# Kernel tuning notes

Hardware: AMD Instinct MI355X
Metric: run time of the kernel (lower is better)

Reference implementation:

```python
import jax, jax.numpy as jnp
import numpy as np

B, T, C, HS = 4, 4096, 1024, 64


def setup_inputs() -> dict:
    key = jax.random.key(0)
    kx, kq, kk, kv = jax.random.split(key, 4)
    x = jax.random.normal(kx, (B, T, C), dtype=jnp.float32)
    s = 1.0 / np.sqrt(C)
    Wq = jax.random.normal(kq, (C, HS), dtype=jnp.float32) * s
    Wk = jax.random.normal(kk, (C, HS), dtype=jnp.float32) * s
    Wv = jax.random.normal(kv, (C, HS), dtype=jnp.float32) * s
    return {"x": x, "Wq": Wq, "Wk": Wk, "Wv": Wv}


def reference(x, Wq, Wk, Wv):
    # q,k,v: [B, T, HS]
    q = x @ Wq
    k = x @ Wk
    v = x @ Wv
    scale = k.shape[-1] ** -0.5
    # full T x T causal attention scores, as the torch module materializes
    scores = jnp.einsum('bqh,bkh->bqk', q, k) * scale  # [B, T, T]
    t = x.shape[1]
    causal = jnp.tril(jnp.ones((t, t), dtype=bool))
    scores = jnp.where(causal[None, :, :], scores, -jnp.inf)
    wei = jax.nn.softmax(scores, axis=-1)  # dropout = 0.0 (eval)
    out = jnp.einsum('bqk,bkh->bqh', wei, v)  # [B, T, HS]
    return out
```

## Files before the change

kernel.cpp:

```cpp
#include <hip/hip_runtime.h>
#include <math.h>

#define BB 4
#define TT 4096
#define CC 1024
#define HS 64
#define MM (BB*TT)

typedef __attribute__((ext_vector_type(8))) short short8;
typedef __attribute__((ext_vector_type(4))) float f32x4;
typedef __attribute__((ext_vector_type(4))) unsigned short ushort4v;

__device__ __forceinline__ unsigned short f2bf(float f) {
    union { float f; unsigned u; } v; v.f = f;
    return (unsigned short)((v.u + 0x7fffu + ((v.u >> 16) & 1u)) >> 16);
}

__global__ __launch_bounds__(256) void prep_kernel(
    const float* __restrict__ Wq, const float* __restrict__ Wk,
    const float* __restrict__ Wv, unsigned short* __restrict__ Wt)
{
    int id = blockIdx.x * 256 + threadIdx.x;
    if (id < 3 * 64 * 1024) {
        int which = id >> 16;
        int n = (id >> 10) & 63;
        int k = id & 1023;
        const float* W = (which == 0) ? Wq : (which == 1) ? Wk : Wv;
        float v = W[k * 64 + n];
        if (which == 0) v *= 0.125f;
        Wt[id] = f2bf(v);
    }
}

__global__ __launch_bounds__(256) void qkv_mfma(
    const float* __restrict__ x, const unsigned short* __restrict__ Wt,
    unsigned short* __restrict__ qb, unsigned short* __restrict__ kb,
    unsigned short* __restrict__ vT)
{
    const int rt = blockIdx.x;
    __shared__ unsigned short xs[64][72];
    __shared__ unsigned short ws[192][72];

    const int t = threadIdx.x;
    const int w = t >> 6;
    const int lane = t & 63;
    const int quad = lane >> 4;
    const int c = lane & 15;

    float4 xreg[2];
    short8 wreg[6];
    #pragma unroll
    for (int i = 0; i < 2; i++) {
        int idx = t + 256 * i;
        int r = idx >> 4, c4 = (idx & 15) * 4;
        xreg[i] = *(const float4*)(x + (size_t)(rt * 32 + r) * CC + c4);
    }
    #pragma unroll
    for (int i = 0; i < 6; i++) {
        int idx = t + 256 * i;
        int n = idx >> 3, c8 = (idx & 7) * 8;
        wreg[i] = *(const short8*)(Wt + (size_t)n * CC + c8);
    }

    f32x4 acc[2][3];
    #pragma unroll
    for (int mt = 0; mt < 2; mt++)
        #pragma unroll
        for (int j = 0; j < 3; j++) acc[mt][j] = (f32x4){0.f, 0.f, 0.f, 0.f};

    for (int k0 = 0; k0 < CC; k0 += 64) {
        __syncthreads();
        #pragma unroll
        for (int i = 0; i < 2; i++) {
            int idx = t + 256 * i;
            int r = idx >> 4, c4 = (idx & 15) * 4;
            ushort4v p = { f2bf(xreg[i].x), f2bf(xreg[i].y), f2bf(xreg[i].z), f2bf(xreg[i].w) };
            *(ushort4v*)&xs[r][c4] = p;
        }
        #pragma unroll
        for (int i = 0; i < 6; i++) {
            int idx = t + 256 * i;
            int n = idx >> 3, c8 = (idx & 7) * 8;
            *(short8*)&ws[n][c8] = wreg[i];
        }
        if (k0 + 64 < CC) {
            #pragma unroll
            for (int i = 0; i < 2; i++) {
                int idx = t + 256 * i;
                int r = idx >> 4, c4 = (idx & 15) * 4;
                xreg[i] = *(const float4*)(x + (size_t)(rt * 32 + r) * CC + k0 + 64 + c4);
            }
            #pragma unroll
            for (int i = 0; i < 6; i++) {
                int idx = t + 256 * i;
                int n = idx >> 3, c8 = (idx & 7) * 8;
                wreg[i] = *(const short8*)(Wt + (size_t)n * CC + k0 + 64 + c8);
            }
        }
        __syncthreads();
        #pragma unroll
        for (int ks = 0; ks < 2; ks++) {
            short8 af[2], bf[3];
            #pragma unroll
            for (int mt = 0; mt < 2; mt++)
                af[mt] = *(const short8*)&xs[16 * mt + c][ks * 32 + quad * 8];
            #pragma unroll
            for (int j = 0; j < 3; j++)
                bf[j] = *(const short8*)&ws[16 * (w + 4 * j) + c][ks * 32 + quad * 8];
            #pragma unroll
            for (int mt = 0; mt < 2; mt++)
                #pragma unroll
                for (int j = 0; j < 3; j++)
                    acc[mt][j] = __builtin_amdgcn_mfma_f32_16x16x32_bf16(af[mt], bf[j], acc[mt][j], 0, 0, 0);
        }
    }

    __syncthreads();
    unsigned short (*vtb)[72] = xs;
    #pragma unroll
    for (int mt = 0; mt < 2; mt++) {
        int grow = rt * 32 + 16 * mt + quad * 4;
        #pragma unroll
        for (int reg = 0; reg < 4; reg++) {
            qb[(size_t)(grow + reg) * HS + 16 * w + c] = f2bf(acc[mt][0][reg]);
            kb[(size_t)(grow + reg) * HS + 16 * w + c] = f2bf(acc[mt][1][reg]);
            vtb[16 * w + c][16 * mt + quad * 4 + reg] = f2bf(acc[mt][2][reg]);
        }
    }
    __syncthreads();
    {
        const int b  = rt >> 7;
        const int t0 = (rt & 127) * 32;
        int d = t >> 2, c8 = (t & 3) * 8;
        short8 v0 = *(const short8*)&vtb[d][c8];
        *(short8*)(vT + (size_t)b * HS * TT + (size_t)d * TT + t0 + c8) = v0;
    }
}

__global__ __launch_bounds__(256) void attn_mfma(
    const unsigned short* __restrict__ qb, const unsigned short* __restrict__ kb,
    const unsigned short* __restrict__ vT, float* __restrict__ out)
{
    const int bid = blockIdx.x;
    const int b   = bid & 3;
    const int qt  = (TT / 32 - 1) - (bid >> 2);
    const int qbase = qt * 32;

    __shared__ unsigned short ks[128][72];
    __shared__ unsigned short vt[64][136];
    __shared__ unsigned short ps[4][16][72];
    __shared__ float obuf[2][16][68];
    __shared__ float lbuf[2][16];

    const int t = threadIdx.x;
    const int w = t >> 6;
    const int lane = t & 63;
    const int quad = lane >> 4;
    const int c = lane & 15;
    const int qh = w & 1;
    const int kp = w >> 1;
    const int qrow = qbase + 16 * qh;

    short8 aq[2];
    #pragma unroll
    for (int kstep = 0; kstep < 2; kstep++)
        aq[kstep] = *(const short8*)(qb + (size_t)(b * TT + qrow + c) * HS + kstep * 32 + quad * 8);

    const int ns = qt / 4 + 1;
    const unsigned short* Kb = kb + (size_t)b * TT * HS;
    const unsigned short* Vb = vT + (size_t)b * HS * TT;

    short8 kreg[4], vreg[4];
    #pragma unroll
    for (int i = 0; i < 4; i++) {
        int idx = t + 256 * i;
        int krow = idx >> 3, kc8 = (idx & 7) * 8;
        kreg[i] = *(const short8*)(Kb + (size_t)krow * HS + kc8);
        int vrow = idx >> 4, vc8 = (idx & 15) * 8;
        vreg[i] = *(const short8*)(Vb + (size_t)vrow * TT + vc8);
    }

    float l[4] = {0.f, 0.f, 0.f, 0.f};
    f32x4 oacc[4];
    #pragma unroll
    for (int dt = 0; dt < 4; dt++) oacc[dt] = (f32x4){0.f, 0.f, 0.f, 0.f};

    for (int s = 0; s < ns; s++) {
        __syncthreads();
        #pragma unroll
        for (int i = 0; i < 4; i++) {
            int idx = t + 256 * i;
            int krow = idx >> 3, kc8 = (idx & 7) * 8;
            *(short8*)&ks[krow][kc8] = kreg[i];
            int vrow = idx >> 4, vc8 = (idx & 15) * 8;
            *(short8*)&vt[vrow][vc8] = vreg[i];
        }
        if (s + 1 < ns) {
            const int base = 128 * (s + 1);
            #pragma unroll
            for (int i = 0; i < 4; i++) {
                int idx = t + 256 * i;
                int krow = idx >> 3, kc8 = (idx & 7) * 8;
                kreg[i] = *(const short8*)(Kb + (size_t)(base + krow) * HS + kc8);
                int vrow = idx >> 4, vc8 = (idx & 15) * 8;
                vreg[i] = *(const short8*)(Vb + (size_t)vrow * TT + base + vc8);
            }
        }
        __syncthreads();

        const int kt0 = 128 * s + 64 * kp;
        if (kt0 <= qbase + 31) {
            f32x4 sc[4];
            #pragma unroll
            for (int st = 0; st < 4; st++) sc[st] = (f32x4){0.f, 0.f, 0.f, 0.f};
            #pragma unroll
            for (int kstep = 0; kstep < 2; kstep++) {
                #pragma unroll
                for (int st = 0; st < 4; st++) {
                    short8 bf = *(const short8*)&ks[64 * kp + 16 * st + c][kstep * 32 + quad * 8];
                    sc[st] = __builtin_amdgcn_mfma_f32_16x16x32_bf16(aq[kstep], bf, sc[st], 0, 0, 0);
                }
            }
            if (kt0 + 63 >= qrow) {
                #pragma unroll
                for (int st = 0; st < 4; st++)
                    #pragma unroll
                    for (int reg = 0; reg < 4; reg++) {
                        int kg = kt0 + 16 * st + c;
                        int qg = qrow + quad * 4 + reg;
                        float p = (kg <= qg) ? __expf(sc[st][reg]) : 0.f;
                        sc[st][reg] = p;
                        l[reg] += p;
                    }
            } else {
                #pragma unroll
                for (int st = 0; st < 4; st++)
                    #pragma unroll
                    for (int reg = 0; reg < 4; reg++) {
                        float p = __expf(sc[st][reg]);
                        sc[st][reg] = p;
                        l[reg] += p;
                    }
            }
            #pragma unroll
            for (int st = 0; st < 4; st++)
                #pragma unroll
                for (int reg = 0; reg < 4; reg++)
                    ps[w][quad * 4 + reg][16 * st + c] = f2bf(sc[st][reg]);

            #pragma unroll
            for (int kstep = 0; kstep < 2; kstep++) {
                short8 ap = *(const short8*)&ps[w][c][kstep * 32 + quad * 8];
                #pragma unroll
                for (int dt = 0; dt < 4; dt++) {
                    short8 bv = *(const short8*)&vt[16 * dt + c][64 * kp + kstep * 32 + quad * 8];
                    oacc[dt] = __builtin_amdgcn_mfma_f32_16x16x32_bf16(ap, bv, oacc[dt], 0, 0, 0);
                }
            }
        }
    }

    #pragma unroll
    for (int reg = 0; reg < 4; reg++)
        #pragma unroll
        for (int msk = 1; msk < 16; msk <<= 1)
            l[reg] += __shfl_xor(l[reg], msk);

    if (kp == 1) {
        #pragma unroll
        for (int dt = 0; dt < 4; dt++)
            #pragma unroll
            for (int reg = 0; reg < 4; reg++)
                obuf[qh][quad * 4 + reg][16 * dt + c] = oacc[dt][reg];
        if (c == 0)
            #pragma unroll
            for (int reg = 0; reg < 4; reg++)
                lbuf[qh][quad * 4 + reg] = l[reg];
    }
    __syncthreads();
    if (kp == 0) {
        float inv[4];
        #pragma unroll
        for (int reg = 0; reg < 4; reg++)
            inv[reg] = 1.f / (l[reg] + lbuf[qh][quad * 4 + reg]);
        #pragma unroll
        for (int dt = 0; dt < 4; dt++)
            #pragma unroll
            for (int reg = 0; reg < 4; reg++) {
                float o = oacc[dt][reg] + obuf[qh][quad * 4 + reg][16 * dt + c];
                out[(size_t)(b * TT + qrow + quad * 4 + reg) * HS + 16 * dt + c] = o * inv[reg];
            }
    }
}

extern "C" void kernel_launch(void* const* d_in, const int* in_sizes, int n_in,
                              void* d_out, int out_size, void* d_ws, size_t ws_size,
                              hipStream_t stream) {
    const float* x  = (const float*)d_in[0];
    const float* Wq = (const float*)d_in[1];
    const float* Wk = (const float*)d_in[2];
    const float* Wv = (const float*)d_in[3];
    float* out = (float*)d_out;

    unsigned short* Wt = (unsigned short*)d_ws;
    unsigned short* qbuf = Wt + 3 * 64 * 1024;
    unsigned short* kbuf = qbuf + (size_t)MM * HS;
    unsigned short* vTb  = kbuf + (size_t)MM * HS;

    prep_kernel<<<768, 256, 0, stream>>>(Wq, Wk, Wv, Wt);
    qkv_mfma<<<MM / 32, 256, 0, stream>>>(x, Wt, qbuf, kbuf, vTb);
    attn_mfma<<<BB * (TT / 32), 256, 0, stream>>>(qbuf, kbuf, vTb, out);
}
```

Before: 150.2 us.

## Split attention over key tiles with partial outputs and a combine kernel

```diff
diff --git a/kernel.cpp b/kernel.cpp
--- a/kernel.cpp
+++ b/kernel.cpp
@@ -20,26 +20,35 @@
     const float* __restrict__ Wq, const float* __restrict__ Wk,
     const float* __restrict__ Wv, unsigned short* __restrict__ Wt)
 {
-    int id = blockIdx.x * 256 + threadIdx.x;
-    if (id < 3 * 64 * 1024) {
-        int which = id >> 16;
-        int n = (id >> 10) & 63;
-        int k = id & 1023;
-        const float* W = (which == 0) ? Wq : (which == 1) ? Wk : Wv;
-        float v = W[k * 64 + n];
-        if (which == 0) v *= 0.125f;
-        Wt[id] = f2bf(v);
-    }
-}
-
-__global__ __launch_bounds__(256) void qkv_mfma(
+    const int which = blockIdx.x >> 4;
+    const int k0 = (blockIdx.x & 15) * 64;
+    const float* __restrict__ W = (which == 0) ? Wq : (which == 1) ? Wk : Wv;
+    const float scale = (which == 0) ? 0.125f : 1.0f;
+    __shared__ unsigned short lds[64][65];
+    const int t = threadIdx.x;
+    #pragma unroll
+    for (int i = 0; i < 16; i++) {
+        int idx = t + 256 * i;
+        int r = idx >> 6, n = idx & 63;
+        lds[r][n] = f2bf(W[(size_t)(k0 + r) * 64 + n] * scale);
+    }
+    __syncthreads();
+    #pragma unroll
+    for (int i = 0; i < 16; i++) {
+        int idx = t + 256 * i;
+        int n = idx >> 6, r = idx & 63;
+        Wt[(which << 16) + (n << 10) + k0 + r] = lds[r][n];
+    }
+}
+
+__global__ __launch_bounds__(256, 2) void qkv_mfma(
     const float* __restrict__ x, const unsigned short* __restrict__ Wt,
     unsigned short* __restrict__ qb, unsigned short* __restrict__ kb,
     unsigned short* __restrict__ vT)
 {
     const int rt = blockIdx.x;
-    __shared__ unsigned short xs[64][72];
-    __shared__ unsigned short ws[192][72];
+    __shared__ unsigned short xs[32][136];
+    __shared__ unsigned short ws[192][136];
 
     const int t = threadIdx.x;
     const int w = t >> 6;
@@ -47,18 +56,18 @@
     const int quad = lane >> 4;
     const int c = lane & 15;
 
-    float4 xreg[2];
-    short8 wreg[6];
-    #pragma unroll
-    for (int i = 0; i < 2; i++) {
+    float4 xreg[4];
+    short8 wreg[12];
+    #pragma unroll
+    for (int i = 0; i < 4; i++) {
         int idx = t + 256 * i;
-        int r = idx >> 4, c4 = (idx & 15) * 4;
+        int r = idx >> 5, c4 = (idx & 31) * 4;
         xreg[i] = *(const float4*)(x + (size_t)(rt * 32 + r) * CC + c4);
     }
     #pragma unroll
-    for (int i = 0; i < 6; i++) {
+    for (int i = 0; i < 12; i++) {
         int idx = t + 256 * i;
-        int n = idx >> 3, c8 = (idx & 7) * 8;
+        int n = idx >> 4, c8 = (idx & 15) * 8;
         wreg[i] = *(const short8*)(Wt + (size_t)n * CC + c8);
     }
 
@@ -68,38 +77,38 @@
         #pragma unroll
         for (int j = 0; j < 3; j++) acc[mt][j] = (f32x4){0.f, 0.f, 0.f, 0.f};
 
-    for (int k0 = 0; k0 < CC; k0 += 64) {
+    for (int k0 = 0; k0 < CC; k0 += 128) {
         __syncthreads();
         #pragma unroll
-        for (int i = 0; i < 2; i++) {
+        for (int i = 0; i < 4; i++) {
             int idx = t + 256 * i;
-            int r = idx >> 4, c4 = (idx & 15) * 4;
+            int r = idx >> 5, c4 = (idx & 31) * 4;
             ushort4v p = { f2bf(xreg[i].x), f2bf(xreg[i].y), f2bf(xreg[i].z), f2bf(xreg[i].w) };
             *(ushort4v*)&xs[r][c4] = p;
         }
         #pragma unroll
-        for (int i = 0; i < 6; i++) {
+        for (int i = 0; i < 12; i++) {
             int idx = t + 256 * i;
-            int n = idx >> 3, c8 = (idx & 7) * 8;
+            int n = idx >> 4, c8 = (idx & 15) * 8;
             *(short8*)&ws[n][c8] = wreg[i];
         }
-        if (k0 + 64 < CC) {
-            #pragma unroll
-            for (int i = 0; i < 2; i++) {
+        if (k0 + 128 < CC) {
+            #pragma unroll
+            for (int i = 0; i < 4; i++) {
                 int idx = t + 256 * i;
-                int r = idx >> 4, c4 = (idx & 15) * 4;
-                xreg[i] = *(const float4*)(x + (size_t)(rt * 32 + r) * CC + k0 + 64 + c4);
-            }
-            #pragma unroll
-            for (int i = 0; i < 6; i++) {
+                int r = idx >> 5, c4 = (idx & 31) * 4;
+                xreg[i] = *(const float4*)(x + (size_t)(rt * 32 + r) * CC + k0 + 128 + c4);
+            }
+            #pragma unroll
+            for (int i = 0; i < 12; i++) {
                 int idx = t + 256 * i;
-                int n = idx >> 3, c8 = (idx & 7) * 8;
-                wreg[i] = *(const short8*)(Wt + (size_t)n * CC + k0 + 64 + c8);
+                int n = idx >> 4, c8 = (idx & 15) * 8;
+                wreg[i] = *(const short8*)(Wt + (size_t)n * CC + k0 + 128 + c8);
             }
         }
         __syncthreads();
         #pragma unroll
-        for (int ks = 0; ks < 2; ks++) {
+        for (int ks = 0; ks < 4; ks++) {
             short8 af[2], bf[3];
             #pragma unroll
             for (int mt = 0; mt < 2; mt++)
@@ -116,7 +125,7 @@
     }
 
     __syncthreads();
-    unsigned short (*vtb)[72] = xs;
+    unsigned short (*vtb)[72] = (unsigned short (*)[72])ws;
     #pragma unroll
     for (int mt = 0; mt < 2; mt++) {
         int grow = rt * 32 + 16 * mt + quad * 4;
@@ -137,47 +146,47 @@
     }
 }
 
-__global__ __launch_bounds__(256) void attn_mfma(
+__global__ __launch_bounds__(256, 4) void attn_mfma(
     const unsigned short* __restrict__ qb, const unsigned short* __restrict__ kb,
-    const unsigned short* __restrict__ vT, float* __restrict__ out)
+    const unsigned short* __restrict__ vT, float* __restrict__ Opart,
+    float* __restrict__ lpart)
 {
     const int bid = blockIdx.x;
-    const int b   = bid & 3;
-    const int qt  = (TT / 32 - 1) - (bid >> 2);
-    const int qbase = qt * 32;
-
-    __shared__ unsigned short ks[128][72];
-    __shared__ unsigned short vt[64][136];
+    const int qt = (TT / 64 - 1) - (bid >> 4);
+    const int j  = (bid >> 2) & 3;
+    const int b  = bid & 3;
+
+    __shared__ unsigned short ks[64][72];
+    __shared__ unsigned short vt[64][72];
     __shared__ unsigned short ps[4][16][72];
-    __shared__ float obuf[2][16][68];
-    __shared__ float lbuf[2][16];
 
     const int t = threadIdx.x;
     const int w = t >> 6;
     const int lane = t & 63;
     const int quad = lane >> 4;
     const int c = lane & 15;
-    const int qh = w & 1;
-    const int kp = w >> 1;
-    const int qrow = qbase + 16 * qh;
+    const int qrow = qt * 64 + 16 * w;
 
     short8 aq[2];
     #pragma unroll
     for (int kstep = 0; kstep < 2; kstep++)
         aq[kstep] = *(const short8*)(qb + (size_t)(b * TT + qrow + c) * HS + kstep * 32 + quad * 8);
 
-    const int ns = qt / 4 + 1;
+    const int nkt = (qt >= j) ? ((qt - j) >> 2) + 1 : 0;
     const unsigned short* Kb = kb + (size_t)b * TT * HS;
     const unsigned short* Vb = vT + (size_t)b * HS * TT;
 
-    short8 kreg[4], vreg[4];
-    #pragma unroll
-    for (int i = 0; i < 4; i++) {
-        int idx = t + 256 * i;
-        int krow = idx >> 3, kc8 = (idx & 7) * 8;
-        kreg[i] = *(const short8*)(Kb + (size_t)krow * HS + kc8);
-        int vrow = idx >> 4, vc8 = (idx & 15) * 8;
-        vreg[i] = *(const short8*)(Vb + (size_t)vrow * TT + vc8);
+    const int srow = t >> 3;
+    const int sc8  = (t & 7) * 8;
+
+    short8 kreg[2], vreg[2];
+    if (nkt > 0) {
+        const int kt0 = j * 64;
+        #pragma unroll
+        for (int i = 0; i < 2; i++) {
+            kreg[i] = *(const short8*)(Kb + (size_t)(kt0 + srow + 32 * i) * HS + sc8);
+            vreg[i] = *(const short8*)(Vb + (size_t)(srow + 32 * i) * TT + kt0 + sc8);
+        }
     }
 
     float l[4] = {0.f, 0.f, 0.f, 0.f};
@@ -185,77 +194,70 @@
     #pragma unroll
     for (int dt = 0; dt < 4; dt++) oacc[dt] = (f32x4){0.f, 0.f, 0.f, 0.f};
 
-    for (int s = 0; s < ns; s++) {
+    for (int i = 0; i < nkt; i++) {
+        const int kt = j + 4 * i;
+        const int kt0 = kt * 64;
         __syncthreads();
         #pragma unroll
-        for (int i = 0; i < 4; i++) {
-            int idx = t + 256 * i;
-            int krow = idx >> 3, kc8 = (idx & 7) * 8;
-            *(short8*)&ks[krow][kc8] = kreg[i];
-            int vrow = idx >> 4, vc8 = (idx & 15) * 8;
-            *(short8*)&vt[vrow][vc8] = vreg[i];
-        }
-        if (s + 1 < ns) {
-            const int base = 128 * (s + 1);
-            #pragma unroll
-            for (int i = 0; i < 4; i++) {
-                int idx = t + 256 * i;
-                int krow = idx >> 3, kc8 = (idx & 7) * 8;
-                kreg[i] = *(const short8*)(Kb + (size_t)(base + krow) * HS + kc8);
-                int vrow = idx >> 4, vc8 = (idx & 15) * 8;
-                vreg[i] = *(const short8*)(Vb + (size_t)vrow * TT + base + vc8);
+        for (int ii = 0; ii < 2; ii++) {
+            *(short8*)&ks[srow + 32 * ii][sc8] = kreg[ii];
+            *(short8*)&vt[srow + 32 * ii][sc8] = vreg[ii];
+        }
+        if (i + 1 < nkt) {
+            const int nb = kt0 + 256;
+            #pragma unroll
+            for (int ii = 0; ii < 2; ii++) {
+                kreg[ii] = *(const short8*)(Kb + (size_t)(nb + srow + 32 * ii) * HS + sc8);
+                vreg[ii] = *(const short8*)(Vb + (size_t)(srow + 32 * ii) * TT + nb + sc8);
             }
         }
         __syncthreads();
 
-        const int kt0 = 128 * s + 64 * kp;
-        if (kt0 <= qbase + 31) {
-            f32x4 sc[4];
-            #pragma unroll
-            for (int st = 0; st < 4; st++) sc[st] = (f32x4){0.f, 0.f, 0.f, 0.f};
-            #pragma unroll
-            for (int kstep = 0; kstep < 2; kstep++) {
-                #pragma unroll
-                for (int st = 0; st < 4; st++) {
-                    short8 bf = *(const short8*)&ks[64 * kp + 16 * st + c][kstep * 32 + quad * 8];
-                    sc[st] = __builtin_amdgcn_mfma_f32_16x16x32_bf16(aq[kstep], bf, sc[st], 0, 0, 0);
-                }
-            }
-            if (kt0 + 63 >= qrow) {
-                #pragma unroll
-                for (int st = 0; st < 4; st++)
-                    #pragma unroll
-                    for (int reg = 0; reg < 4; reg++) {
-                        int kg = kt0 + 16 * st + c;
-                        int qg = qrow + quad * 4 + reg;
-                        float p = (kg <= qg) ? __expf(sc[st][reg]) : 0.f;
-                        sc[st][reg] = p;
-                        l[reg] += p;
-                    }
-            } else {
-                #pragma unroll
-                for (int st = 0; st < 4; st++)
-                    #pragma unroll
-                    for (int reg = 0; reg < 4; reg++) {
-                        float p = __expf(sc[st][reg]);
-                        sc[st][reg] = p;
-                        l[reg] += p;
-                    }
-            }
+        f32x4 sc[4];
+        #pragma unroll
+        for (int st = 0; st < 4; st++) sc[st] = (f32x4){0.f, 0.f, 0.f, 0.f};
+        #pragma unroll
+        for (int kstep = 0; kstep < 2; kstep++) {
+            #pragma unroll
+            for (int st = 0; st < 4; st++) {
+                short8 bf = *(const short8*)&ks[16 * st + c][kstep * 32 + quad * 8];
+                sc[st] = __builtin_amdgcn_mfma_f32_16x16x32_bf16(aq[kstep], bf, sc[st], 0, 0, 0);
+            }
+        }
+        if (kt == qt) {
             #pragma unroll
             for (int st = 0; st < 4; st++)
                 #pragma unroll
-                for (int reg = 0; reg < 4; reg++)
-                    ps[w][quad * 4 + reg][16 * st + c] = f2bf(sc[st][reg]);
-
-            #pragma unroll
-            for (int kstep = 0; kstep < 2; kstep++) {
-                short8 ap = *(const short8*)&ps[w][c][kstep * 32 + quad * 8];
+                for (int reg = 0; reg < 4; reg++) {
+                    int kg = kt0 + 16 * st + c;
+                    int qg = qrow + quad * 4 + reg;
+                    float p = (kg <= qg) ? __expf(sc[st][reg]) : 0.f;
+                    sc[st][reg] = p;
+                    l[reg] += p;
+                }
+        } else {
+            #pragma unroll
+            for (int st = 0; st < 4; st++)
                 #pragma unroll
-                for (int dt = 0; dt < 4; dt++) {
-                    short8 bv = *(const short8*)&vt[16 * dt + c][64 * kp + kstep * 32 + quad * 8];
-                    oacc[dt] = __builtin_amdgcn_mfma_f32_16x16x32_bf16(ap, bv, oacc[dt], 0, 0, 0);
+                for (int reg = 0; reg < 4; reg++) {
+                    float p = __expf(sc[st][reg]);
+                    sc[st][reg] = p;
+                    l[reg] += p;
                 }
+        }
+        #pragma unroll
+        for (int st = 0; st < 4; st++)
+            #pragma unroll
+            for (int reg = 0; reg < 4; reg++)
+                ps[w][quad * 4 + reg][16 * st + c] = f2bf(sc[st][reg]);
+
+        #pragma unroll
+        for (int kstep = 0; kstep < 2; kstep++) {
+            short8 ap = *(const short8*)&ps[w][c][kstep * 32 + quad * 8];
+            #pragma unroll
+            for (int dt = 0; dt < 4; dt++) {
+                short8 bv = *(const short8*)&vt[16 * dt + c][kstep * 32 + quad * 8];
+                oacc[dt] = __builtin_amdgcn_mfma_f32_16x16x32_bf16(ap, bv, oacc[dt], 0, 0, 0);
             }
         }
     }
@@ -266,31 +268,35 @@
         for (int msk = 1; msk < 16; msk <<= 1)
             l[reg] += __shfl_xor(l[reg], msk);
 
-    if (kp == 1) {
-        #pragma unroll
-        for (int dt = 0; dt < 4; dt++)
-            #pragma unroll
-            for (int reg = 0; reg < 4; reg++)
-                obuf[qh][quad * 4 + reg][16 * dt + c] = oacc[dt][reg];
-        if (c == 0)
-            #pragma unroll
-            for (int reg = 0; reg < 4; reg++)
-                lbuf[qh][quad * 4 + reg] = l[reg];
-    }
-    __syncthreads();
-    if (kp == 0) {
-        float inv[4];
+    float* __restrict__ Oj = Opart + (size_t)j * MM * HS;
+    #pragma unroll
+    for (int dt = 0; dt < 4; dt++)
         #pragma unroll
         for (int reg = 0; reg < 4; reg++)
-            inv[reg] = 1.f / (l[reg] + lbuf[qh][quad * 4 + reg]);
-        #pragma unroll
-        for (int dt = 0; dt < 4; dt++)
-            #pragma unroll
-            for (int reg = 0; reg < 4; reg++) {
-                float o = oacc[dt][reg] + obuf[qh][quad * 4 + reg][16 * dt + c];
-                out[(size_t)(b * TT + qrow + quad * 4 + reg) * HS + 16 * dt + c] = o * inv[reg];
-            }
-    }
+            Oj[(size_t)(b * TT + qrow + quad * 4 + reg) * HS + 16 * dt + c] = oacc[dt][reg];
+    if (c == 0)
+        #pragma unroll
+        for (int reg = 0; reg < 4; reg++)
+            lpart[(size_t)j * MM + b * TT + qrow + quad * 4 + reg] = l[reg];
+}
+
+__global__ __launch_bounds__(256) void combine_kernel(
+    const float* __restrict__ Opart, const float* __restrict__ lpart,
+    float* __restrict__ out)
+{
+    const int id = blockIdx.x * 256 + threadIdx.x;
+    const int row = id >> 4;
+    float l = lpart[row] + lpart[MM + row] + lpart[2 * MM + row] + lpart[3 * MM + row];
+    const float4* O = (const float4*)Opart;
+    const size_t stride = (size_t)MM * HS / 4;
+    float4 a = O[id], b = O[id + stride], c = O[id + 2 * stride], d = O[id + 3 * stride];
+    float inv = 1.f / l;
+    float4 r;
+    r.x = (a.x + b.x + c.x + d.x) * inv;
+    r.y = (a.y + b.y + c.y + d.y) * inv;
+    r.z = (a.z + b.z + c.z + d.z) * inv;
+    r.w = (a.w + b.w + c.w + d.w) * inv;
+    ((float4*)out)[id] = r;
 }
 
 extern "C" void kernel_launch(void* const* d_in, const int* in_sizes, int n_in,
@@ -302,12 +308,15 @@
     const float* Wv = (const float*)d_in[3];
     float* out = (float*)d_out;
 
-    unsigned short* Wt = (unsigned short*)d_ws;
+    unsigned short* Wt   = (unsigned short*)d_ws;
     unsigned short* qbuf = Wt + 3 * 64 * 1024;
     unsigned short* kbuf = qbuf + (size_t)MM * HS;
     unsigned short* vTb  = kbuf + (size_t)MM * HS;
-
-    prep_kernel<<<768, 256, 0, stream>>>(Wq, Wk, Wv, Wt);
+    float* Opart = (float*)(vTb + (size_t)MM * HS);
+    float* lpart = Opart + 4 * (size_t)MM * HS;
+
+    prep_kernel<<<48, 256, 0, stream>>>(Wq, Wk, Wv, Wt);
     qkv_mfma<<<MM / 32, 256, 0, stream>>>(x, Wt, qbuf, kbuf, vTb);
-    attn_mfma<<<BB * (TT / 32), 256, 0, stream>>>(qbuf, kbuf, vTb, out);
-}
+    attn_mfma<<<BB * (TT / 64) * 4, 256, 0, stream>>>(qbuf, kbuf, vTb, Opart, lpart);
+    combine_kernel<<<1024, 256, 0, stream>>>(Opart, lpart, out);
+}
```

Result: faster. 136.6 us (-9.0%).
